# Kernel tuning notes

Measured on AMD Instinct MI355X. Metric: run time of the kernel, lower is better.

The kernel has to match this reference:

```python
import jax, jax.numpy as jnp
import numpy as np


def setup_inputs() -> dict:
    key = jax.random.key(0)
    ks = jax.random.split(key, 7)
    T, B, X, H = 256, 64, 512, 2048
    s_ih = 1.0 / np.sqrt(H)
    return {
        "input": jax.random.normal(ks[0], (T, B, X), dtype=jnp.float32),
        "h_0": jax.random.normal(ks[1], (B, H), dtype=jnp.float32),
        "c_0": jax.random.normal(ks[2], (B, H), dtype=jnp.float32),
        "w_ih": jax.random.normal(ks[3], (4 * H, X), dtype=jnp.float32) * s_ih,
        "w_hh": jax.random.normal(ks[4], (4 * H, H), dtype=jnp.float32) * s_ih,
        "b_ih": jax.random.normal(ks[5], (4 * H,), dtype=jnp.float32) * s_ih,
        "b_hh": jax.random.normal(ks[6], (4 * H,), dtype=jnp.float32) * s_ih,
    }


def reference(input, h_0, c_0, w_ih, w_hh, b_ih, b_hh):
    H = h_0.shape[-1]
    # Precompute input projections for all timesteps in one big GEMM: [T,B,4H]
    x_proj = jnp.einsum("tbx,gx->tbg", input, w_ih) + b_ih + b_hh

    def step(carry, xg):
        h, c = carry
        gates = xg + h @ w_hh.T  # [B, 4H]
        i, f, g, o = jnp.split(gates, 4, axis=-1)  # torch LSTMCell gate order
        i = jax.nn.sigmoid(i)
        f = jax.nn.sigmoid(f)
        g = jnp.tanh(g)
        o = jax.nn.sigmoid(o)
        c_new = f * c + i * g
        h_new = o * jnp.tanh(c_new)
        y = jax.nn.softmax(h_new, axis=-1)  # per-step softmax over hidden dim
        return (h_new, c_new), y

    (h_T, c_T), ys = jax.lax.scan(step, (h_0, c_0), x_proj)
    return ys, h_T, c_T
```

## Files before the change

kernel.cpp:

```cpp
#include <hip/hip_runtime.h>

#define Tn 256
#define Bn 64
#define Xn 512
#define Hn 2048
#define Gn 8192
#define NWG 256

typedef short bf16x8 __attribute__((ext_vector_type(8)));
typedef float f32x4 __attribute__((ext_vector_type(4)));
typedef unsigned uint32x4 __attribute__((ext_vector_type(4)));

#define AL(p)    __hip_atomic_load((p), __ATOMIC_RELAXED, __HIP_MEMORY_SCOPE_AGENT)
#define AS(p, v) __hip_atomic_store((p), (v), __ATOMIC_RELAXED, __HIP_MEMORY_SCOPE_AGENT)
#define AADD(p, v) __hip_atomic_fetch_add((p), (v), __ATOMIC_RELAXED, __HIP_MEMORY_SCOPE_AGENT)

static __device__ __forceinline__ unsigned short f2bf(float f) {
    unsigned int u = __builtin_bit_cast(unsigned int, f);
    u += 0x7fffu + ((u >> 16) & 1u);
    return (unsigned short)(u >> 16);
}
static __device__ __forceinline__ float bf2f(unsigned short s) {
    unsigned int u = ((unsigned int)s) << 16;
    return __builtin_bit_cast(float, u);
}
static __device__ __forceinline__ void cvt4(const float* __restrict__ s,
                                            unsigned short* __restrict__ d, int i) {
    float4 v = ((const float4*)s)[i];
    ushort4 o;
    o.x = f2bf(v.x); o.y = f2bf(v.y); o.z = f2bf(v.z); o.w = f2bf(v.w);
    ((ushort4*)d)[i] = o;
}
static __device__ __forceinline__ float sigm(float x) {
    return 1.f / (1.f + __expf(-x));
}
static __device__ __forceinline__ float ftanh(float x) {
    float e = __expf(2.f * x);
    return (e - 1.f) / (e + 1.f);
}

template <int RING>
static __device__ __forceinline__ size_t hoff(int t) {
    if constexpr (RING) return (size_t)((t * 97) % 257) * 262144;
    else                return (size_t)(t & 1) * 262144;
}
template <int RING>
static __device__ __forceinline__ bf16x8 ldh(const unsigned short* p) {
    if constexpr (RING) {
        return *(const bf16x8*)p;
    } else {
        unsigned* q = (unsigned*)p;
        uint32x4 v;
        v[0] = AL(q + 0); v[1] = AL(q + 1); v[2] = AL(q + 2); v[3] = AL(q + 3);
        return __builtin_bit_cast(bf16x8, v);
    }
}
template <int RING>
static __device__ __forceinline__ float ldh1(const unsigned short* hb, int idx) {
    if constexpr (RING) {
        return bf2f(hb[idx]);
    } else {
        unsigned d = AL((unsigned*)(hb + (idx & ~1)));
        return bf2f((idx & 1) ? (unsigned short)(d >> 16) : (unsigned short)(d & 0xffffu));
    }
}

static __device__ __forceinline__ void pair_wait(unsigned* sh, int s0, int s1,
                                                 unsigned target, int l) {
    if (!target) return;
    unsigned* p = sh + ((l == 0) ? s0 : s1) * 16;
    for (;;) {
        unsigned a = AL(p);
        if (__all(a >= target)) break;
        __builtin_amdgcn_s_sleep(1);
    }
}

__global__ void prologue3(const float* __restrict__ x, const float* __restrict__ h0,
                          const float* __restrict__ b_ih, const float* __restrict__ b_hh,
                          const float* __restrict__ w_ih,
                          unsigned short* __restrict__ Xb, unsigned short* __restrict__ XFrag,
                          unsigned short* __restrict__ hb0, float* __restrict__ bias,
                          unsigned* __restrict__ flags)
{
    int i = blockIdx.x * blockDim.x + threadIdx.x;
    const int n_x  = Tn * Bn * Xn / 4;
    const int n_xf = Gn * Xn / 4;
    const int n_h  = Bn * Hn / 4;
    const int n_b  = Gn / 4;
    if (i < n_x) { cvt4(x, Xb, i); return; }
    i -= n_x;
    if (i < n_xf) {
        int wg = i >> 12, r = i & 4095;
        int c = r >> 7, k = (r & 127) * 4;
        int g = c >> 3, u = c & 7;
        float4 v = *(const float4*)(w_ih + (size_t)(g * Hn + wg * 8 + u) * Xn + k);
        ushort4 o;
        o.x = f2bf(v.x); o.y = f2bf(v.y); o.z = f2bf(v.z); o.w = f2bf(v.w);
        int ct = c >> 4, kk = k >> 5, l = ((k >> 3) & 3) * 16 + (c & 15);
        *(ushort4*)((char*)XFrag + (size_t)wg * 32768 + (size_t)((ct * 16 + kk) * 64 + l) * 16 + (k & 7) * 2) = o;
        return;
    }
    i -= n_xf;
    if (i < n_h) {
        int flat = i * 4;
        int row = flat >> 11, unit0 = flat & 2047;
        float4 v = ((const float4*)h0)[i];
        ushort4 o;
        o.x = f2bf(v.x); o.y = f2bf(v.y); o.z = f2bf(v.z); o.w = f2bf(v.w);
        int dst = (((unit0 >> 3) << 6) + row) * 8 + (unit0 & 7);
        *(ushort4*)(hb0 + dst) = o;
        return;
    }
    i -= n_h;
    if (i < n_b) {
        float4 a = ((const float4*)b_ih)[i];
        float4 b = ((const float4*)b_hh)[i];
        ((float4*)bias)[i] = make_float4(a.x + b.x, a.y + b.y, a.z + b.z, a.w + b.w);
        return;
    }
    i -= n_b;
    if (i < 256) flags[i] = 0u;
}

#define MFMA4(a0v, a1v) \
    acc00 = __builtin_amdgcn_mfma_f32_16x16x32_bf16((a0v), b0, acc00, 0, 0, 0); \
    acc10 = __builtin_amdgcn_mfma_f32_16x16x32_bf16((a1v), b0, acc10, 0, 0, 0); \
    acc01 = __builtin_amdgcn_mfma_f32_16x16x32_bf16((a0v), b1, acc01, 0, 0, 0); \
    acc11 = __builtin_amdgcn_mfma_f32_16x16x32_bf16((a1v), b1, acc11, 0, 0, 0);

template <int RING>
__global__ __launch_bounds__(512, 2) void lstm_persist5(
    const unsigned short* __restrict__ Xb, const unsigned short* __restrict__ XFrag,
    const float* __restrict__ bias, const float* __restrict__ c0,
    char* __restrict__ hbase, const float* __restrict__ w_hh,
    float* __restrict__ ys, float* __restrict__ hT, float* __restrict__ cT,
    unsigned* __restrict__ shards)
{
    extern __shared__ char smem[];
    const unsigned short* LW = (const unsigned short*)smem;
    float* RED  = (float*)(smem + 131072);
    float* RED2 = (float*)(smem + 155648);

    const int wg  = blockIdx.x;
    const int tid = threadIdx.x;
    const int U0  = wg * 8;

    for (int i = tid; i < 32 * 512; i += 512) {
        int c = i >> 9, k = (i & 511) * 4;
        int g = c >> 3, u = c & 7;
        float4 v = *(const float4*)(w_hh + (size_t)(g * Hn + U0 + u) * Hn + k);
        ushort4 o;
        o.x = f2bf(v.x); o.y = f2bf(v.y); o.z = f2bf(v.z); o.w = f2bf(v.w);
        int ct = c >> 4, kk = k >> 5, l = ((k >> 3) & 3) * 16 + (c & 15);
        *(ushort4*)(smem + ((size_t)((ct * 64 + kk) * 64 + l) * 16 + (k & 7) * 2)) = o;
    }
    __syncthreads();

    const int w = tid >> 6, l = tid & 63;
    const int lm = l & 15, lh = l >> 4;
    const int kh = w >> 1, rblk = w & 1, rb = rblk * 32;
    const int kk0 = kh * 16;
    const int kx0 = kh * 4;

    const int u  = lm & 15 & 7;
    const bool hi = (lm & 8) != 0;

    float bi = 0.f, bf_ = 0.f, bg = 0.f, bo = 0.f;
    float cs[2][2] = {{0.f, 0.f}, {0.f, 0.f}};
    if (kh == 0) {
        bi  = bias[0 * Hn + U0 + u];
        bf_ = bias[1 * Hn + U0 + u];
        bg  = bias[2 * Hn + U0 + u];
        bo  = bias[3 * Hn + U0 + u];
        #pragma unroll
        for (int s = 0; s < 2; ++s)
            #pragma unroll
            for (int j = 0; j < 2; ++j)
                cs[s][j] = c0[(size_t)(rb + s * 16 + 4 * lh + (hi ? 2 : 0) + j) * Hn + U0 + u];
    }

    const char* xfb = (const char*)XFrag + (size_t)wg * 32768;
    const int srb = w - 2;

    for (int t = 0; t < Tn; ++t) {
        const unsigned short* hb = (const unsigned short*)(hbase + hoff<RING>(t));
        unsigned short* hn = (unsigned short*)(hbase + hoff<RING>(t + 1));

        f32x4 acc00 = {0,0,0,0}, acc01 = {0,0,0,0}, acc10 = {0,0,0,0}, acc11 = {0,0,0,0};

        {
            const unsigned short* xa0 = Xb + (size_t)(t * 64 + rb + lm) * Xn + lh * 8;
            const unsigned short* xa1 = xa0 + 16 * Xn;
            bf16x8 xA0[4], xA1[4];
            #pragma unroll
            for (int j = 0; j < 4; ++j) {
                xA0[j] = *(const bf16x8*)(xa0 + (kx0 + j) * 32);
                xA1[j] = *(const bf16x8*)(xa1 + (kx0 + j) * 32);
            }
            #pragma unroll
            for (int kkl = 0; kkl < 4; ++kkl) {
                bf16x8 b0 = *(const bf16x8*)(xfb + ((size_t)((0 * 16 + kx0 + kkl) * 64 + l) << 4));
                bf16x8 b1 = *(const bf16x8*)(xfb + ((size_t)((1 * 16 + kx0 + kkl) * 64 + l) << 4));
                MFMA4(xA0[kkl], xA1[kkl]);
            }
        }

        pair_wait(shards, 2 * kh, 2 * kh + 1, (unsigned)t * 32u, l);

        {
            const unsigned short* ha0 = hb + (size_t)(rb + lm) * 8;
            const unsigned short* ha1 = ha0 + 128;
            bf16x8 aP0[4], aP1[4];
            #pragma unroll
            for (int j = 0; j < 4; ++j) {
                int g = (kk0 + j) * 4 + lh;
                aP0[j] = ldh<RING>(ha0 + (size_t)g * 512);
                aP1[j] = ldh<RING>(ha1 + (size_t)g * 512);
            }
            #pragma unroll 4
            for (int kkl = 0; kkl < 16; ++kkl) {
                bf16x8 a0v = aP0[kkl & 3], a1v = aP1[kkl & 3];
                if (kkl < 12) {
                    int g = (kk0 + kkl + 4) * 4 + lh;
                    aP0[kkl & 3] = ldh<RING>(ha0 + (size_t)g * 512);
                    aP1[kkl & 3] = ldh<RING>(ha1 + (size_t)g * 512);
                }
                bf16x8 b0 = *(const bf16x8*)(LW + ((size_t)((0 * 64 + kk0 + kkl) * 64 + l) << 3));
                bf16x8 b1 = *(const bf16x8*)(LW + ((size_t)((1 * 64 + kk0 + kkl) * 64 + l) << 3));
                MFMA4(a0v, a1v);
            }
        }

        const bool do_sm = (srb >= 0 && srb < 4) && (wg < Bn) && (t > 0);
        float sv[8];
        if (kh != 0) {
            int slot = (kh - 1) * 2 + rblk;
            int base = (slot * 64 + l) * 4;
            *(f32x4*)(RED + 0 * 1536 + base) = acc00;
            *(f32x4*)(RED + 1 * 1536 + base) = acc01;
            *(f32x4*)(RED + 2 * 1536 + base) = acc10;
            *(f32x4*)(RED + 3 * 1536 + base) = acc11;
            if (do_sm) {
                pair_wait(shards, 2 * srb, 2 * srb + 1, (unsigned)t * 32u, l);
                int row = wg;
                float m = -1e30f;
                #pragma unroll
                for (int j = 0; j < 8; ++j) {
                    int uu = srb * 512 + j * 64 + l;
                    sv[j] = ldh1<RING>(hb, (uu >> 3) * 512 + row * 8 + (uu & 7));
                    m = fmaxf(m, sv[j]);
                }
                #pragma unroll
                for (int off = 32; off; off >>= 1) m = fmaxf(m, __shfl_xor(m, off));
                float s = 0.f;
                #pragma unroll
                for (int j = 0; j < 8; ++j) s += __expf(sv[j] - m);
                #pragma unroll
                for (int off = 32; off; off >>= 1) s += __shfl_xor(s, off);
                if (l == 0) { RED2[srb * 2] = m; RED2[srb * 2 + 1] = s; }
            }
        }
        __syncthreads();

        if (kh == 0) {
            #pragma unroll
            for (int p = 0; p < 3; ++p) {
                int base = ((p * 2 + rblk) * 64 + l) * 4;
                acc00 += *(const f32x4*)(RED + 0 * 1536 + base);
                acc01 += *(const f32x4*)(RED + 1 * 1536 + base);
                acc10 += *(const f32x4*)(RED + 2 * 1536 + base);
                acc11 += *(const f32x4*)(RED + 3 * 1536 + base);
            }
            f32x4 sA[2], sB[2];
            #pragma unroll
            for (int r = 0; r < 4; ++r) {
                sA[0][r] = __shfl_xor(acc00[r], 8); sB[0][r] = __shfl_xor(acc01[r], 8);
                sA[1][r] = __shfl_xor(acc10[r], 8); sB[1][r] = __shfl_xor(acc11[r], 8);
            }
            #pragma unroll
            for (int s = 0; s < 2; ++s) {
                f32x4 aA = s ? acc10 : acc00;
                f32x4 aB = s ? acc11 : acc01;
                #pragma unroll
                for (int j = 0; j < 2; ++j) {
                    int r = (hi ? 2 : 0) + j;
                    float gi = (hi ? sA[s][r] : aA[r]) + bi;
                    float gf = (hi ? aA[r] : sA[s][r]) + bf_;
                    float gg = (hi ? sB[s][r] : aB[r]) + bg;
                    float go = (hi ? aB[r] : sB[s][r]) + bo;
                    float iv = sigm(gi), fv = sigm(gf), gv = ftanh(gg), ov = sigm(go);
                    float cc = cs[s][j];
                    float cn = fv * cc + iv * gv;
                    float hv = ov * ftanh(cn);
                    cs[s][j] = cn;
                    int rowg = rb + s * 16 + 4 * lh + (hi ? 2 : 0) + j;
                    unsigned short mybf = f2bf(hv);
                    unsigned other = (unsigned)__shfl_xor((int)(unsigned)mybf, 1);
                    if (!(u & 1)) {
                        AS((unsigned*)(hn + (size_t)wg * 512 + rowg * 8 + u),
                           (unsigned)mybf | (other << 16));
                    }
                    if (t == Tn - 1) {
                        size_t off = (size_t)rowg * Hn + U0 + u;
                        hT[off] = hv;
                        cT[off] = cn;
                    }
                }
            }
        }
        __syncthreads();
        if (tid == 0) AADD(shards + (wg >> 5) * 16, 1u);

        if (do_sm) {
            float m0 = RED2[0], sA0 = RED2[1], m1 = RED2[2], sB0 = RED2[3];
            float m2 = RED2[4], sC0 = RED2[5], m3 = RED2[6], sD0 = RED2[7];
            float gm = fmaxf(fmaxf(m0, m1), fmaxf(m2, m3));
            float gs = sA0 * __expf(m0 - gm) + sB0 * __expf(m1 - gm) +
                       sC0 * __expf(m2 - gm) + sD0 * __expf(m3 - gm);
            float inv = 1.f / gs;
            float* yr = ys + ((size_t)(t - 1) * Bn + wg) * Hn + srb * 512;
            #pragma unroll
            for (int j = 0; j < 8; ++j) yr[j * 64 + l] = __expf(sv[j] - gm) * inv;
        }
    }

    {
        const unsigned short* hfin = (const unsigned short*)(hbase + hoff<RING>(Tn));
        const bool act = (srb >= 0 && srb < 4) && (wg < Bn);
        float sv[8];
        if (act) {
            pair_wait(shards, 2 * srb, 2 * srb + 1, (unsigned)Tn * 32u, l);
            int row = wg;
            float m = -1e30f;
            #pragma unroll
            for (int j = 0; j < 8; ++j) {
                int uu = srb * 512 + j * 64 + l;
                sv[j] = ldh1<RING>(hfin, (uu >> 3) * 512 + row * 8 + (uu & 7));
                m = fmaxf(m, sv[j]);
            }
            #pragma unroll
            for (int off = 32; off; off >>= 1) m = fmaxf(m, __shfl_xor(m, off));
            float s = 0.f;
            #pragma unroll
            for (int j = 0; j < 8; ++j) s += __expf(sv[j] - m);
            #pragma unroll
            for (int off = 32; off; off >>= 1) s += __shfl_xor(s, off);
            if (l == 0) { RED2[srb * 2] = m; RED2[srb * 2 + 1] = s; }
        }
        __syncthreads();
        if (act) {
            float m0 = RED2[0], sA0 = RED2[1], m1 = RED2[2], sB0 = RED2[3];
            float m2 = RED2[4], sC0 = RED2[5], m3 = RED2[6], sD0 = RED2[7];
            float gm = fmaxf(fmaxf(m0, m1), fmaxf(m2, m3));
            float gs = sA0 * __expf(m0 - gm) + sB0 * __expf(m1 - gm) +
                       sC0 * __expf(m2 - gm) + sD0 * __expf(m3 - gm);
            float inv = 1.f / gs;
            float* yr = ys + ((size_t)(Tn - 1) * Bn + wg) * Hn + srb * 512;
            #pragma unroll
            for (int j = 0; j < 8; ++j) yr[j * 64 + l] = __expf(sv[j] - gm) * inv;
        }
    }
}

extern "C" void kernel_launch(void* const* d_in, const int* in_sizes, int n_in,
                              void* d_out, int out_size, void* d_ws, size_t ws_size,
                              hipStream_t stream) {
    const float* input = (const float*)d_in[0];
    const float* h0    = (const float*)d_in[1];
    const float* c0    = (const float*)d_in[2];
    const float* w_ih  = (const float*)d_in[3];
    const float* w_hh  = (const float*)d_in[4];
    const float* b_ih  = (const float*)d_in[5];
    const float* b_hh  = (const float*)d_in[6];

    float* ys = (float*)d_out;
    float* hT = ys + (size_t)Tn * Bn * Hn;
    float* cT = hT + (size_t)Bn * Hn;

    char* wsb = (char*)d_ws;
    unsigned short* Xb  = (unsigned short*)wsb;
    unsigned short* XF  = (unsigned short*)(wsb + 16777216);
    float* bias         = (float*)(wsb + 25165824);
    unsigned* flags     = (unsigned*)(wsb + 25198592);
    char* hbase         = wsb + 25199616;
    const size_t need_ring = 25199616 + (size_t)257 * 262144;

    const int prol_items = Tn * Bn * Xn / 4 + Gn * Xn / 4 + Bn * Hn / 4 + Gn / 4 + 256;
    const int prol_blocks = (prol_items + 255) / 256;
    prologue3<<<dim3(prol_blocks), dim3(256), 0, stream>>>(
        input, h0, b_ih, b_hh, w_ih, Xb, XF, (unsigned short*)hbase, bias, flags);

    if (ws_size >= need_ring) {
        (void)hipFuncSetAttribute((const void*)lstm_persist5<1>,
                                  hipFuncAttributeMaxDynamicSharedMemorySize, 155680);
        lstm_persist5<1><<<dim3(NWG), dim3(512), 155680, stream>>>(
            Xb, XF, bias, c0, hbase, w_hh, ys, hT, cT, flags);
    } else {
        (void)hipFuncSetAttribute((const void*)lstm_persist5<0>,
                                  hipFuncAttributeMaxDynamicSharedMemorySize, 155680);
        lstm_persist5<0><<<dim3(NWG), dim3(512), 155680, stream>>>(
            Xb, XF, bias, c0, hbase, w_hh, ys, hT, cT, flags);
    }
}
```

Baseline: 1.958 ms.

## Replace sharded atomic counters with per-workgroup step flags and finer waits

Inter-workgroup sync moves from atomic-add shard counters to per-workgroup, per-row-block step flags. Each wave polls only the 64 flags it depends on and writes its own flag right after its h stores drain, which removes the block-wide barrier before signalling. The h-operand prefetch depth doubles from 4 to 8 registers and launch bounds drop to one block per SM, giving more registers for the deeper prefetch. The risk is that polling 64 flags per wave costs more memory traffic than polling one counter, and the relaxed store after the vmcnt wait leans on ordering that is not formally guaranteed.

```diff
diff --git a/kernel.cpp b/kernel.cpp
--- a/kernel.cpp
+++ b/kernel.cpp
@@ -13,7 +13,6 @@
 
 #define AL(p)    __hip_atomic_load((p), __ATOMIC_RELAXED, __HIP_MEMORY_SCOPE_AGENT)
 #define AS(p, v) __hip_atomic_store((p), (v), __ATOMIC_RELAXED, __HIP_MEMORY_SCOPE_AGENT)
-#define AADD(p, v) __hip_atomic_fetch_add((p), (v), __ATOMIC_RELAXED, __HIP_MEMORY_SCOPE_AGENT)
 
 static __device__ __forceinline__ unsigned short f2bf(float f) {
     unsigned int u = __builtin_bit_cast(unsigned int, f);
@@ -65,15 +64,10 @@
     }
 }
 
-static __device__ __forceinline__ void pair_wait(unsigned* sh, int s0, int s1,
-                                                 unsigned target, int l) {
-    if (!target) return;
-    unsigned* p = sh + ((l == 0) ? s0 : s1) * 16;
-    for (;;) {
-        unsigned a = AL(p);
-        if (__all(a >= target)) break;
-        __builtin_amdgcn_s_sleep(1);
-    }
+static __device__ __forceinline__ void flags_wait64(const unsigned* f, unsigned t, int l) {
+    if (!t) return;
+    const unsigned* p = f + l;
+    while (!__all(AL(p) >= t)) __builtin_amdgcn_s_sleep(1);
 }
 
 __global__ void prologue3(const float* __restrict__ x, const float* __restrict__ h0,
@@ -120,7 +114,7 @@
         return;
     }
     i -= n_b;
-    if (i < 256) flags[i] = 0u;
+    if (i < 512) flags[i] = 0u;
 }
 
 #define MFMA4(a0v, a1v) \
@@ -130,12 +124,12 @@
     acc11 = __builtin_amdgcn_mfma_f32_16x16x32_bf16((a1v), b1, acc11, 0, 0, 0);
 
 template <int RING>
-__global__ __launch_bounds__(512, 2) void lstm_persist5(
+__global__ __launch_bounds__(512, 1) void lstm_persist6(
     const unsigned short* __restrict__ Xb, const unsigned short* __restrict__ XFrag,
     const float* __restrict__ bias, const float* __restrict__ c0,
     char* __restrict__ hbase, const float* __restrict__ w_hh,
     float* __restrict__ ys, float* __restrict__ hT, float* __restrict__ cT,
-    unsigned* __restrict__ shards)
+    unsigned* __restrict__ flags)
 {
     extern __shared__ char smem[];
     const unsigned short* LW = (const unsigned short*)smem;
@@ -163,7 +157,7 @@
     const int kk0 = kh * 16;
     const int kx0 = kh * 4;
 
-    const int u  = lm & 15 & 7;
+    const int u  = lm & 7;
     const bool hi = (lm & 8) != 0;
 
     float bi = 0.f, bf_ = 0.f, bg = 0.f, bo = 0.f;
@@ -182,6 +176,8 @@
 
     const char* xfb = (const char*)XFrag + (size_t)wg * 32768;
     const int srb = w - 2;
+    const unsigned* gate_f = flags + (rblk ? 256 : 0) + kh * 64;
+    const unsigned* sm_f   = flags + (wg < 32 ? 0 : 256) + (srb & 3) * 64;
 
     for (int t = 0; t < Tn; ++t) {
         const unsigned short* hb = (const unsigned short*)(hbase + hoff<RING>(t));
@@ -206,25 +202,25 @@
             }
         }
 
-        pair_wait(shards, 2 * kh, 2 * kh + 1, (unsigned)t * 32u, l);
+        flags_wait64(gate_f, (unsigned)t, l);
 
         {
             const unsigned short* ha0 = hb + (size_t)(rb + lm) * 8;
             const unsigned short* ha1 = ha0 + 128;
-            bf16x8 aP0[4], aP1[4];
-            #pragma unroll
-            for (int j = 0; j < 4; ++j) {
+            bf16x8 aP0[8], aP1[8];
+            #pragma unroll
+            for (int j = 0; j < 8; ++j) {
                 int g = (kk0 + j) * 4 + lh;
                 aP0[j] = ldh<RING>(ha0 + (size_t)g * 512);
                 aP1[j] = ldh<RING>(ha1 + (size_t)g * 512);
             }
-            #pragma unroll 4
+            #pragma unroll
             for (int kkl = 0; kkl < 16; ++kkl) {
-                bf16x8 a0v = aP0[kkl & 3], a1v = aP1[kkl & 3];
-                if (kkl < 12) {
-                    int g = (kk0 + kkl + 4) * 4 + lh;
-                    aP0[kkl & 3] = ldh<RING>(ha0 + (size_t)g * 512);
-                    aP1[kkl & 3] = ldh<RING>(ha1 + (size_t)g * 512);
+                bf16x8 a0v = aP0[kkl & 7], a1v = aP1[kkl & 7];
+                if (kkl < 8) {
+                    int g = (kk0 + kkl + 8) * 4 + lh;
+                    aP0[kkl & 7] = ldh<RING>(ha0 + (size_t)g * 512);
+                    aP1[kkl & 7] = ldh<RING>(ha1 + (size_t)g * 512);
                 }
                 bf16x8 b0 = *(const bf16x8*)(LW + ((size_t)((0 * 64 + kk0 + kkl) * 64 + l) << 3));
                 bf16x8 b1 = *(const bf16x8*)(LW + ((size_t)((1 * 64 + kk0 + kkl) * 64 + l) << 3));
@@ -242,7 +238,7 @@
             *(f32x4*)(RED + 2 * 1536 + base) = acc10;
             *(f32x4*)(RED + 3 * 1536 + base) = acc11;
             if (do_sm) {
-                pair_wait(shards, 2 * srb, 2 * srb + 1, (unsigned)t * 32u, l);
+                flags_wait64(sm_f, (unsigned)t, l);
                 int row = wg;
                 float m = -1e30f;
                 #pragma unroll
@@ -308,11 +304,9 @@
                     }
                 }
             }
-        }
-        __syncthreads();
-        if (tid == 0) AADD(shards + (wg >> 5) * 16, 1u);
-
-        if (do_sm) {
+            asm volatile("s_waitcnt vmcnt(0)" ::: "memory");
+            if (l == 0) AS(flags + (rblk ? 256 : 0) + wg, (unsigned)(t + 1));
+        } else if (do_sm) {
             float m0 = RED2[0], sA0 = RED2[1], m1 = RED2[2], sB0 = RED2[3];
             float m2 = RED2[4], sC0 = RED2[5], m3 = RED2[6], sD0 = RED2[7];
             float gm = fmaxf(fmaxf(m0, m1), fmaxf(m2, m3));
@@ -323,6 +317,7 @@
             #pragma unroll
             for (int j = 0; j < 8; ++j) yr[j * 64 + l] = __expf(sv[j] - gm) * inv;
         }
+        __syncthreads();
     }
 
     {
@@ -330,7 +325,7 @@
         const bool act = (srb >= 0 && srb < 4) && (wg < Bn);
         float sv[8];
         if (act) {
-            pair_wait(shards, 2 * srb, 2 * srb + 1, (unsigned)Tn * 32u, l);
+            flags_wait64(sm_f, (unsigned)Tn, l);
             int row = wg;
             float m = -1e30f;
             #pragma unroll
@@ -383,23 +378,23 @@
     unsigned short* XF  = (unsigned short*)(wsb + 16777216);
     float* bias         = (float*)(wsb + 25165824);
     unsigned* flags     = (unsigned*)(wsb + 25198592);
-    char* hbase         = wsb + 25199616;
-    const size_t need_ring = 25199616 + (size_t)257 * 262144;
-
-    const int prol_items = Tn * Bn * Xn / 4 + Gn * Xn / 4 + Bn * Hn / 4 + Gn / 4 + 256;
+    char* hbase         = wsb + 25200640;
+    const size_t need_ring = 25200640 + (size_t)257 * 262144;
+
+    const int prol_items = Tn * Bn * Xn / 4 + Gn * Xn / 4 + Bn * Hn / 4 + Gn / 4 + 512;
     const int prol_blocks = (prol_items + 255) / 256;
     prologue3<<<dim3(prol_blocks), dim3(256), 0, stream>>>(
         input, h0, b_ih, b_hh, w_ih, Xb, XF, (unsigned short*)hbase, bias, flags);
 
     if (ws_size >= need_ring) {
-        (void)hipFuncSetAttribute((const void*)lstm_persist5<1>,
+        (void)hipFuncSetAttribute((const void*)lstm_persist6<1>,
                                   hipFuncAttributeMaxDynamicSharedMemorySize, 155680);
-        lstm_persist5<1><<<dim3(NWG), dim3(512), 155680, stream>>>(
+        lstm_persist6<1><<<dim3(NWG), dim3(512), 155680, stream>>>(
             Xb, XF, bias, c0, hbase, w_hh, ys, hT, cT, flags);
     } else {
-        (void)hipFuncSetAttribute((const void*)lstm_persist5<0>,
+        (void)hipFuncSetAttribute((const void*)lstm_persist6<0>,
                                   hipFuncAttributeMaxDynamicSharedMemorySize, 155680);
-        lstm_persist5<0><<<dim3(NWG), dim3(512), 155680, stream>>>(
+        lstm_persist6<0><<<dim3(NWG), dim3(512), 155680, stream>>>(
             Xb, XF, bias, c0, hbase, w_hh, ys, hT, cT, flags);
     }
 }
```

Result: slower. 2.235 ms (+14.2%).

## Use finer-grained per-row-block arrival flags and drop block barrier before signaling

Applied to the files above, without the earlier changes.

Replaces the per-32-workgroup shard counters with per-8-workgroup counters split by row block, so each wave waits only on the eight groups that produced the slice of h it reads. Each writing wave now drains its own stores and signals directly, instead of waiting on a block-wide __syncthreads followed by one thread incrementing. The goal is less over-waiting and a shorter critical path per timestep in the persistent recurrence. In exchange the flag array and workspace offsets grow, more atomics are issued, and correctness now depends on the vmcnt drain being a sufficient release.

```diff
diff --git a/kernel.cpp b/kernel.cpp
--- a/kernel.cpp
+++ b/kernel.cpp
@@ -65,12 +65,12 @@
     }
 }
 
-static __device__ __forceinline__ void pair_wait(unsigned* sh, int s0, int s1,
-                                                 unsigned target, int l) {
+static __device__ __forceinline__ void oct_wait(const unsigned* sh, int base,
+                                                unsigned target, int l) {
     if (!target) return;
-    unsigned* p = sh + ((l == 0) ? s0 : s1) * 16;
+    const unsigned* p = sh + (base + (l & 7)) * 16;
     for (;;) {
-        unsigned a = AL(p);
+        unsigned a = (l < 8) ? AL(p) : target;
         if (__all(a >= target)) break;
         __builtin_amdgcn_s_sleep(1);
     }
@@ -120,7 +120,7 @@
         return;
     }
     i -= n_b;
-    if (i < 256) flags[i] = 0u;
+    if (i < 1024) flags[i] = 0u;
 }
 
 #define MFMA4(a0v, a1v) \
@@ -130,12 +130,12 @@
     acc11 = __builtin_amdgcn_mfma_f32_16x16x32_bf16((a1v), b1, acc11, 0, 0, 0);
 
 template <int RING>
-__global__ __launch_bounds__(512, 2) void lstm_persist5(
+__global__ __launch_bounds__(512, 2) void lstm_persist7(
     const unsigned short* __restrict__ Xb, const unsigned short* __restrict__ XFrag,
     const float* __restrict__ bias, const float* __restrict__ c0,
     char* __restrict__ hbase, const float* __restrict__ w_hh,
     float* __restrict__ ys, float* __restrict__ hT, float* __restrict__ cT,
-    unsigned* __restrict__ shards)
+    unsigned* __restrict__ flags)
 {
     extern __shared__ char smem[];
     const unsigned short* LW = (const unsigned short*)smem;
@@ -163,7 +163,7 @@
     const int kk0 = kh * 16;
     const int kx0 = kh * 4;
 
-    const int u  = lm & 15 & 7;
+    const int u  = lm & 7;
     const bool hi = (lm & 8) != 0;
 
     float bi = 0.f, bf_ = 0.f, bg = 0.f, bo = 0.f;
@@ -182,6 +182,8 @@
 
     const char* xfb = (const char*)XFrag + (size_t)wg * 32768;
     const int srb = w - 2;
+    const unsigned* gate_f = flags + rblk * 512;
+    const unsigned* sm_f   = flags + (wg < 32 ? 0 : 512);
 
     for (int t = 0; t < Tn; ++t) {
         const unsigned short* hb = (const unsigned short*)(hbase + hoff<RING>(t));
@@ -206,7 +208,7 @@
             }
         }
 
-        pair_wait(shards, 2 * kh, 2 * kh + 1, (unsigned)t * 32u, l);
+        oct_wait(gate_f, kh * 8, (unsigned)t * 8u, l);
 
         {
             const unsigned short* ha0 = hb + (size_t)(rb + lm) * 8;
@@ -242,7 +244,7 @@
             *(f32x4*)(RED + 2 * 1536 + base) = acc10;
             *(f32x4*)(RED + 3 * 1536 + base) = acc11;
             if (do_sm) {
-                pair_wait(shards, 2 * srb, 2 * srb + 1, (unsigned)t * 32u, l);
+                oct_wait(sm_f, srb * 8, (unsigned)t * 8u, l);
                 int row = wg;
                 float m = -1e30f;
                 #pragma unroll
@@ -308,11 +310,9 @@
                     }
                 }
             }
-        }
-        __syncthreads();
-        if (tid == 0) AADD(shards + (wg >> 5) * 16, 1u);
-
-        if (do_sm) {
+            asm volatile("s_waitcnt vmcnt(0)" ::: "memory");
+            if (l == 0) AADD((unsigned*)(flags + rblk * 512 + (wg >> 3) * 16), 1u);
+        } else if (do_sm) {
             float m0 = RED2[0], sA0 = RED2[1], m1 = RED2[2], sB0 = RED2[3];
             float m2 = RED2[4], sC0 = RED2[5], m3 = RED2[6], sD0 = RED2[7];
             float gm = fmaxf(fmaxf(m0, m1), fmaxf(m2, m3));
@@ -323,6 +323,7 @@
             #pragma unroll
             for (int j = 0; j < 8; ++j) yr[j * 64 + l] = __expf(sv[j] - gm) * inv;
         }
+        __syncthreads();
     }
 
     {
@@ -330,7 +331,7 @@
         const bool act = (srb >= 0 && srb < 4) && (wg < Bn);
         float sv[8];
         if (act) {
-            pair_wait(shards, 2 * srb, 2 * srb + 1, (unsigned)Tn * 32u, l);
+            oct_wait(sm_f, srb * 8, (unsigned)Tn * 8u, l);
             int row = wg;
             float m = -1e30f;
             #pragma unroll
@@ -383,23 +384,23 @@
     unsigned short* XF  = (unsigned short*)(wsb + 16777216);
     float* bias         = (float*)(wsb + 25165824);
     unsigned* flags     = (unsigned*)(wsb + 25198592);
-    char* hbase         = wsb + 25199616;
-    const size_t need_ring = 25199616 + (size_t)257 * 262144;
-
-    const int prol_items = Tn * Bn * Xn / 4 + Gn * Xn / 4 + Bn * Hn / 4 + Gn / 4 + 256;
+    char* hbase         = wsb + 25202688;
+    const size_t need_ring = 25202688 + (size_t)257 * 262144;
+
+    const int prol_items = Tn * Bn * Xn / 4 + Gn * Xn / 4 + Bn * Hn / 4 + Gn / 4 + 1024;
     const int prol_blocks = (prol_items + 255) / 256;
     prologue3<<<dim3(prol_blocks), dim3(256), 0, stream>>>(
         input, h0, b_ih, b_hh, w_ih, Xb, XF, (unsigned short*)hbase, bias, flags);
 
     if (ws_size >= need_ring) {
-        (void)hipFuncSetAttribute((const void*)lstm_persist5<1>,
+        (void)hipFuncSetAttribute((const void*)lstm_persist7<1>,
                                   hipFuncAttributeMaxDynamicSharedMemorySize, 155680);
-        lstm_persist5<1><<<dim3(NWG), dim3(512), 155680, stream>>>(
+        lstm_persist7<1><<<dim3(NWG), dim3(512), 155680, stream>>>(
             Xb, XF, bias, c0, hbase, w_hh, ys, hT, cT, flags);
     } else {
-        (void)hipFuncSetAttribute((const void*)lstm_persist5<0>,
+        (void)hipFuncSetAttribute((const void*)lstm_persist7<0>,
                                   hipFuncAttributeMaxDynamicSharedMemorySize, 155680);
-        lstm_persist5<0><<<dim3(NWG), dim3(512), 155680, stream>>>(
+        lstm_persist7<0><<<dim3(NWG), dim3(512), 155680, stream>>>(
             Xb, XF, bias, c0, hbase, w_hh, ys, hT, cT, flags);
     }
 }
```

Result: no change. 1.963 ms (+0.3%).
